# Optimization experiments

Measured on AMD Instinct MI355X. Metric: run time of the kernel, lower is better.

The kernel has to match this reference:

```python
import jax, jax.numpy as jnp
import numpy as np


def setup_inputs() -> dict:
    key = jax.random.key(0)
    kq, kk, kv = jax.random.split(key, 3)
    B, H, S, D = 2, 16, 2048, 64
    return {
        "queries": jax.random.normal(kq, (B, H, S, D), dtype=jnp.float32),
        "keys": jax.random.normal(kk, (B, H, S, D), dtype=jnp.float32),
        "values": jax.random.normal(kv, (B, H, S, D), dtype=jnp.float32),
        "d_k": D,
    }


def reference(queries, keys, values, d_k):
    # scores = Q K^T / sqrt(d_k)  -> [B, H, S, S]
    scale = 1.0 / jnp.sqrt(jnp.asarray(d_k, dtype=queries.dtype))
    scores = jnp.einsum("bhqd,bhkd->bhqk", queries, keys) * scale
    weights = jax.nn.softmax(scores, axis=-1)
    return jnp.einsum("bhqk,bhkd->bhqd", weights, values)
```

## Files before the change

### kernel.cpp

```cpp
#include <hip/hip_runtime.h>


typedef _Float16 half8 __attribute__((ext_vector_type(8)));
typedef _Float16 half4 __attribute__((ext_vector_type(4)));
typedef __fp16 fp16x2 __attribute__((ext_vector_type(2)));
typedef float floatx4 __attribute__((ext_vector_type(4)));

constexpr int BQ = 64;
constexpr int BK = 64;
constexpr int DH = 64;
constexpr int SLEN = 2048;
constexpr int NT = SLEN / BK;
constexpr int THREADS = 256;

#define MFMA16(a, b, c) __builtin_amdgcn_mfma_f32_16x16x32_f16(a, b, c, 0, 0, 0)

static __device__ __forceinline__ void load_lds16(const _Float16* g, _Float16* l) {
    __builtin_amdgcn_global_load_lds(
        (const __attribute__((address_space(1))) void*)g,
        (__attribute__((address_space(3))) void*)l, 16, 0, 0);
}

__global__ __launch_bounds__(256)
void prep_frags(const float* __restrict__ K, const float* __restrict__ V,
                _Float16* __restrict__ F)
{
    __shared__ _Float16 kt_[64 * 72];
    __shared__ _Float16 vt_[64 * 72];
    const int tid  = threadIdx.x;
    const int tile = blockIdx.x & 31;
    const int head = blockIdx.x >> 5;
    const size_t base = ((size_t)head * SLEN + tile * 64) * DH;
    const float4* Ks = (const float4*)(K + base);
    const float4* Vs = (const float4*)(V + base);
    #pragma unroll
    for (int r = 0; r < 4; r++) {
        int i = tid + 256 * r, row = i >> 4, g = i & 15;
        float4 a = Ks[row * 16 + g];
        half4 h;
        h[0] = (_Float16)a.x; h[1] = (_Float16)a.y;
        h[2] = (_Float16)a.z; h[3] = (_Float16)a.w;
        *(half4*)&kt_[row * 72 + g * 4] = h;
        float4 b = Vs[row * 16 + g];
        half4 h2;
        h2[0] = (_Float16)b.x; h2[1] = (_Float16)b.y;
        h2[2] = (_Float16)b.z; h2[3] = (_Float16)b.w;
        *(half4*)&vt_[row * 72 + g * 4] = h2;
    }
    __syncthreads();
    _Float16* dst = F + (size_t)(head * 32 + tile) * 8192;
    #pragma unroll
    for (int r = 0; r < 2; r++) {
        int s = tid + 256 * r;
        int frag = s >> 6, lane = s & 63;
        int kd = frag >> 2, c = frag & 3;
        int quad = lane >> 4, n16 = lane & 15;
        int key = (c >> 1) * 32 + (c & 1) * 4 + (n16 >> 2) * 8 + (n16 & 3);
        *(half8*)&dst[s * 8] = *(const half8*)&kt_[key * 72 + kd * 32 + quad * 8];
    }
    #pragma unroll
    for (int r = 0; r < 2; r++) {
        int s = tid + 256 * r;
        int frag = s >> 6, lane = s & 63;
        int kd2 = frag >> 2, c2 = frag & 3;
        int quad = lane >> 4, n16 = lane & 15;
        int d = c2 * 16 + n16;
        int key0 = kd2 * 32 + quad * 8;
        half8 h;
        #pragma unroll
        for (int j = 0; j < 8; j++) h[j] = vt_[(key0 + j) * 72 + d];
        *(half8*)&dst[4096 + s * 8] = h;
    }
}

__global__ __launch_bounds__(THREADS, 4)
void attn_f16_mfma(const float* __restrict__ Q, const _Float16* __restrict__ F,
                   float* __restrict__ Out, const int* __restrict__ dkp)
{
    __shared__ _Float16 lds[2][8192];

    const int tid  = threadIdx.x;
    const int wq   = tid >> 6;
    const int lane = tid & 63;
    const int quad = lane >> 4;
    const int n16  = lane & 15;

    const int id   = blockIdx.x;
    const int xcd  = id & 7;
    const int slot = id >> 3;
    const int head = xcd * 4 + (slot >> 5);
    const int qt   = slot & 31;

    const float scale2 = rsqrtf((float)(*dkp)) * 1.44269504088896340736f;
    const size_t headoff = (size_t)head * SLEN * DH;

    half8 qB[2];
    {
        const float4* Qg = (const float4*)(Q + headoff + (size_t)(qt * BQ + wq * 16) * DH);
        #pragma unroll
        for (int kd = 0; kd < 2; kd++) {
            float4 a = Qg[n16 * 16 + kd * 8 + quad * 2];
            float4 b = Qg[n16 * 16 + kd * 8 + quad * 2 + 1];
            half8 h;
            h[0] = (_Float16)(a.x * scale2); h[1] = (_Float16)(a.y * scale2);
            h[2] = (_Float16)(a.z * scale2); h[3] = (_Float16)(a.w * scale2);
            h[4] = (_Float16)(b.x * scale2); h[5] = (_Float16)(b.y * scale2);
            h[6] = (_Float16)(b.z * scale2); h[7] = (_Float16)(b.w * scale2);
            qB[kd] = h;
        }
    }

    const _Float16* Fh = F + (size_t)head * 32 * 8192;

    auto stage = [&](_Float16* dst, int kt) {
        const _Float16* src = Fh + (size_t)kt * 8192 + wq * 512 + lane * 8;
        #pragma unroll
        for (int i = 0; i < 4; i++)
            load_lds16(src + i * 2048, dst + wq * 512 + i * 2048);
    };

    floatx4 oacc[4];
    floatx4 lsum;
    const floatx4 fz = {0.f, 0.f, 0.f, 0.f};
    lsum = fz;
    #pragma unroll
    for (int c2 = 0; c2 < 4; c2++) oacc[c2] = fz;
    half8 ones;
    #pragma unroll
    for (int j = 0; j < 8; j++) ones[j] = (_Float16)1.0f;

    union PU { fp16x2 h2[4]; half8 h8; };

    auto tile_compute = [&](const _Float16* Bl) {
        const _Float16* Kl = Bl;
        const _Float16* Vl = Bl + 4096;

        half8 kA[2][4];
        #pragma unroll
        for (int kd = 0; kd < 2; kd++)
            #pragma unroll
            for (int c = 0; c < 4; c++)
                kA[kd][c] = *(const half8*)&Kl[((kd * 4 + c) * 64 + lane) * 8];

        floatx4 sC[4];
        #pragma unroll
        for (int c = 0; c < 4; c++) {
            floatx4 acc = MFMA16(kA[0][c], qB[0], fz);
            sC[c] = MFMA16(kA[1][c], qB[1], acc);
        }

        half8 pB[2];
        #pragma unroll
        for (int kd2 = 0; kd2 < 2; kd2++) {
            PU u_;
            u_.h2[0] = __builtin_amdgcn_cvt_pkrtz(exp2f(sC[kd2 * 2][0]),
                                                  exp2f(sC[kd2 * 2][1]));
            u_.h2[1] = __builtin_amdgcn_cvt_pkrtz(exp2f(sC[kd2 * 2][2]),
                                                  exp2f(sC[kd2 * 2][3]));
            u_.h2[2] = __builtin_amdgcn_cvt_pkrtz(exp2f(sC[kd2 * 2 + 1][0]),
                                                  exp2f(sC[kd2 * 2 + 1][1]));
            u_.h2[3] = __builtin_amdgcn_cvt_pkrtz(exp2f(sC[kd2 * 2 + 1][2]),
                                                  exp2f(sC[kd2 * 2 + 1][3]));
            pB[kd2] = u_.h8;
        }

        half8 vA[2][4];
        #pragma unroll
        for (int kd2 = 0; kd2 < 2; kd2++)
            #pragma unroll
            for (int c2 = 0; c2 < 4; c2++)
                vA[kd2][c2] = *(const half8*)&Vl[((kd2 * 4 + c2) * 64 + lane) * 8];

        __builtin_amdgcn_s_setprio(1);
        lsum = MFMA16(ones, pB[0], lsum);
        lsum = MFMA16(ones, pB[1], lsum);
        #pragma unroll
        for (int c2 = 0; c2 < 4; c2++) {
            oacc[c2] = MFMA16(vA[0][c2], pB[0], oacc[c2]);
            oacc[c2] = MFMA16(vA[1][c2], pB[1], oacc[c2]);
        }
        __builtin_amdgcn_s_setprio(0);
    };

    stage(&lds[0][0], 0);

    for (int kt = 0; kt < NT; kt += 2) {
        asm volatile("s_waitcnt vmcnt(0)" ::: "memory");
        __builtin_amdgcn_sched_barrier(0);
        __syncthreads();
        if (kt + 1 < NT) stage(&lds[1][0], kt + 1);
        tile_compute(&lds[0][0]);

        asm volatile("s_waitcnt vmcnt(0)" ::: "memory");
        __builtin_amdgcn_sched_barrier(0);
        __syncthreads();
        if (kt + 2 < NT) stage(&lds[0][0], kt + 2);
        tile_compute(&lds[1][0]);
    }

    float* Og = Out + headoff + (size_t)(qt * BQ + wq * 16) * DH;
    float inv = 1.0f / lsum[0];
    #pragma unroll
    for (int c2 = 0; c2 < 4; c2++) {
        floatx4 v = oacc[c2];
        float4 w = make_float4(v[0] * inv, v[1] * inv, v[2] * inv, v[3] * inv);
        *(float4*)&Og[n16 * DH + c2 * 16 + quad * 4] = w;
    }
}

extern "C" void kernel_launch(void* const* d_in, const int* in_sizes, int n_in,
                              void* d_out, int out_size, void* d_ws, size_t ws_size,
                              hipStream_t stream) {
    const float* Q = (const float*)d_in[0];
    const float* K = (const float*)d_in[1];
    const float* V = (const float*)d_in[2];
    const int*  dk = (const int*)d_in[3];
    float* Out = (float*)d_out;

    const int nbh = in_sizes[0] / (SLEN * DH);

    _Float16* F = (_Float16*)d_ws;

    prep_frags<<<nbh * 32, 256, 0, stream>>>(K, V, F);

    dim3 grid(nbh * (SLEN / BQ));
    attn_f16_mfma<<<grid, THREADS, 0, stream>>>(Q, F, Out, dk);
}
```

Measured before the change: 144.3 us.

## Deepen K/V LDS pipeline to four buffers with partial vmcnt waits

Replaces the double-buffered K/V fragment staging with a four-slot LDS ring that prefetches three tiles ahead. Each step waits only until the oldest tile's loads have landed (vmcnt 8/4/0) instead of draining all loads. The aim is to hide global load latency behind more MFMA work. The cost is doubling LDS use to 64KB and lowering the launch-bounds occupancy hint from 4 to 2 blocks, which reduces the number of waves per CU available for latency hiding.

```diff
diff --git a/kernel.cpp b/kernel.cpp
--- a/kernel.cpp
+++ b/kernel.cpp
@@ -73,11 +73,11 @@
     }
 }
 
-__global__ __launch_bounds__(THREADS, 4)
+__global__ __launch_bounds__(THREADS, 2)
 void attn_f16_mfma(const float* __restrict__ Q, const _Float16* __restrict__ F,
                    float* __restrict__ Out, const int* __restrict__ dkp)
 {
-    __shared__ _Float16 lds[2][8192];
+    __shared__ _Float16 lds[4][8192];
 
     const int tid  = threadIdx.x;
     const int wq   = tid >> 6;
@@ -182,21 +182,34 @@
         __builtin_amdgcn_s_setprio(0);
     };
 
+#define WAITV_(N) asm volatile("s_waitcnt vmcnt(" #N ")" ::: "memory")
+#define WAITV(N) WAITV_(N)
+#define BARRIER_SYNC() do {                                                \
+    __builtin_amdgcn_sched_barrier(0);                                     \
+    __builtin_amdgcn_s_barrier();                                          \
+    __builtin_amdgcn_sched_barrier(0);                                     \
+} while (0)
+#define PBODY(BI, T, VM, DOSTAGE) do {                                     \
+    WAITV(VM);                                                             \
+    BARRIER_SYNC();                                                        \
+    if (DOSTAGE) stage(&lds[((BI) + 3) & 3][0], (T) + 3);                  \
+    tile_compute(&lds[BI][0]);                                             \
+} while (0)
+
     stage(&lds[0][0], 0);
-
-    for (int kt = 0; kt < NT; kt += 2) {
-        asm volatile("s_waitcnt vmcnt(0)" ::: "memory");
-        __builtin_amdgcn_sched_barrier(0);
-        __syncthreads();
-        if (kt + 1 < NT) stage(&lds[1][0], kt + 1);
-        tile_compute(&lds[0][0]);
-
-        asm volatile("s_waitcnt vmcnt(0)" ::: "memory");
-        __builtin_amdgcn_sched_barrier(0);
-        __syncthreads();
-        if (kt + 2 < NT) stage(&lds[0][0], kt + 2);
-        tile_compute(&lds[1][0]);
-    }
+    stage(&lds[1][0], 1);
+    stage(&lds[2][0], 2);
+
+    for (int kt = 0; kt < NT - 4; kt += 4) {
+        PBODY(0, kt,     8, true);
+        PBODY(1, kt + 1, 8, true);
+        PBODY(2, kt + 2, 8, true);
+        PBODY(3, kt + 3, 8, true);
+    }
+    PBODY(0, NT - 4, 8, true);
+    PBODY(1, NT - 3, 8, false);
+    PBODY(2, NT - 2, 4, false);
+    PBODY(3, NT - 1, 0, false);
 
     float* Og = Out + headoff + (size_t)(qt * BQ + wq * 16) * DH;
     float inv = 1.0f / lsum[0];
```

Result: slower. 148.5 us (+2.9%).
